# Kernel optimization log

Hardware: AMD Instinct MI355X
Metric: run time of the kernel (lower is better)

## Reference

```python
import jax, jax.numpy as jnp
import numpy as np

N = 50000   # nodes
E = 400000  # edges
IN = 32     # in_channel
M = 64      # mid_channel
L = 3       # num_layers
EPS = 1e-5


def layer_norm(x, g, b):
    mu = jnp.mean(x, axis=-1, keepdims=True)
    var = jnp.mean((x - mu) ** 2, axis=-1, keepdims=True)
    return (x - mu) / jnp.sqrt(var + EPS) * g + b


def setup_inputs() -> dict:
    key = jax.random.key(0)
    ks = jax.random.split(key, 14)
    s = 0.05
    return {
        "x": jax.random.normal(ks[0], (N, IN), jnp.float32),
        "edge_index": jax.random.randint(ks[1], (2, E), 0, N, jnp.int64),
        # node encoder: Linear(IN->M) + LayerNorm(M)
        "enc_W": jax.random.normal(ks[2], (IN, M), jnp.float32) * s,
        "enc_b": jnp.zeros((M,), jnp.float32),
        "enc_g": jnp.ones((M,), jnp.float32),
        "enc_beta": jnp.zeros((M,), jnp.float32),
        # per-layer pre-norm
        "ln_g": jnp.ones((L, M), jnp.float32),
        "ln_b": jnp.zeros((L, M), jnp.float32),
        # SAGEConvV2 edge MLP: Linear(2M->2M) -> ReLU -> Linear(2M->M)
        "W1": jax.random.normal(ks[3], (L, 2 * M, 2 * M), jnp.float32) * s,
        "b1": jnp.zeros((L, 2 * M), jnp.float32),
        "W2": jax.random.normal(ks[4], (L, 2 * M, M), jnp.float32) * s,
        "b2": jnp.zeros((L, M), jnp.float32),
        # root weight lin_r: Linear(M->M, bias=False)
        "Wr": jax.random.normal(ks[5], (L, M, M), jnp.float32) * s,
    }


def reference(x, edge_index, enc_W, enc_b, enc_g, enc_beta,
              ln_g, ln_b, W1, b1, W2, b2, Wr):
    src = edge_index[0]  # x_j source nodes
    dst = edge_index[1]  # x_i target nodes (aggregation index)
    # node encoder
    x = layer_norm(x @ enc_W + enc_b, enc_g, enc_beta)
    # mean-aggregation denominator (in-degree, clamped to 1 like PyG scatter-mean)
    deg = jax.ops.segment_sum(jnp.ones((E,), x.dtype), dst, num_segments=N)
    deg = jnp.maximum(deg, 1.0)[:, None]
    for l in range(L):  # small fixed layer count
        # res+ block: norm -> act -> (dropout: identity in eval) -> conv -> residual
        h = jax.nn.relu(layer_norm(x, ln_g[l], ln_b[l]))
        # message: concat([x_i, x_j]) -> 2-layer MLP   [E, 2M] -> [E, M]
        msg = jnp.concatenate([h[dst], h[src]], axis=-1)
        msg = jax.nn.relu(msg @ W1[l] + b1[l]) @ W2[l] + b2[l]
        # scatter-mean aggregate at target nodes
        agg = jax.ops.segment_sum(msg, dst, num_segments=N) / deg
        # root weight
        h = agg + h @ Wr[l]
        x = x + h
    return x
```

## Files before the change

kernel.cpp:

```cpp
#include <hip/hip_runtime.h>
#include <hip/hip_bf16.h>

#define N_NODES 50000
#define N_EDGES 400000
#define IN_CH 32
#define EPS 1e-5f
#define SCAN_NB ((N_NODES + 1023) / 1024)
#define EL_CAP 384

#define HIST_B ((N_EDGES + 255) / 256)
#define WCT_TOT (3 * 320 * 64)
#define W2T_TOT (3 * 64 * 128)
#define RPK_B ((WCT_TOT + W2T_TOT + 255) / 256)
#define ENC_B ((N_NODES + 63) / 64)

typedef __attribute__((ext_vector_type(8))) short bh8;
typedef __attribute__((ext_vector_type(4))) float fx4;
typedef __attribute__((ext_vector_type(2))) float fx2;

static __device__ __forceinline__ unsigned int f2bf(float f) {
    __hip_bfloat16 h = __float2bfloat16(f);
    return (unsigned int)*(unsigned short*)&h;
}
static __device__ __forceinline__ unsigned short f2bfu(float f) {
    __hip_bfloat16 h = __float2bfloat16(f);
    return *(unsigned short*)&h;
}
static __device__ __forceinline__ float bflo(unsigned int u) { return __uint_as_float(u << 16); }

__global__ __launch_bounds__(256) void setup_kernel(
    const int* __restrict__ ei, int* __restrict__ cnt,
    const float* __restrict__ W1, const float* __restrict__ Wr,
    const float* __restrict__ W2,
    unsigned short* __restrict__ WcT, unsigned short* __restrict__ W2T,
    const float* __restrict__ x, const float* __restrict__ encW,
    const float* __restrict__ encb, const float* __restrict__ encg,
    const float* __restrict__ encbeta, float* __restrict__ xout) {
    int b = blockIdx.x;
    if (b < HIST_B) {
        int e = b * 256 + threadIdx.x;
        if (e < N_EDGES) atomicAdd(&cnt[ei[N_EDGES + e]], 1);
        return;
    }
    b -= HIST_B;
    if (b < RPK_B) {
        int t = b * 256 + threadIdx.x;
        if (t < WCT_TOT) {
            int l = t / (320 * 64);
            int rem = t % (320 * 64);
            int j = rem / 64, c = rem % 64;
            float v;
            if (j < 128)      v = W1[(l * 128 + c) * 128 + j];
            else if (j < 256) v = W1[(l * 128 + 64 + c) * 128 + (j - 128)];
            else              v = Wr[(l * 64 + c) * 64 + (j - 256)];
            WcT[t] = f2bfu(v);
        } else if (t < WCT_TOT + W2T_TOT) {
            int t2 = t - WCT_TOT;
            int l = t2 / 8192, rem = t2 % 8192;
            int n = rem / 128, k = rem % 128;
            W2T[t2] = f2bfu(W2[l * 8192 + k * 64 + n]);
        }
        return;
    }
    b -= RPK_B;
    __shared__ unsigned short wT[64 * 32];
    int tid = threadIdx.x;
    for (int t = tid; t < IN_CH * 64; t += 256) {
        int k = t >> 6, c = t & 63;
        wT[c * 32 + k] = f2bfu(encW[t]);
    }
    __syncthreads();
    int lane = tid & 63, wid = tid >> 6;
    int l15 = lane & 15, g4 = lane >> 4;
    int node0 = b * 64 + wid * 16;
    int arow = min(node0 + l15, N_NODES - 1);
    float4 xa = *(const float4*)(x + (size_t)arow * 32 + g4 * 8);
    float4 xb = *(const float4*)(x + (size_t)arow * 32 + g4 * 8 + 4);
    bh8 af;
    af[0] = (short)f2bfu(xa.x); af[1] = (short)f2bfu(xa.y);
    af[2] = (short)f2bfu(xa.z); af[3] = (short)f2bfu(xa.w);
    af[4] = (short)f2bfu(xb.x); af[5] = (short)f2bfu(xb.y);
    af[6] = (short)f2bfu(xb.z); af[7] = (short)f2bfu(xb.w);
    float cb[4], gvv[4], bvv[4];
    fx4 cf[4];
    #pragma unroll
    for (int nb = 0; nb < 4; ++nb) {
        int cc = nb * 16 + l15;
        cb[nb] = encb[cc]; gvv[nb] = encg[cc]; bvv[nb] = encbeta[cc];
        bh8 bf = *(const bh8*)&wT[(nb * 16 + l15) * 32 + g4 * 8];
        cf[nb] = __builtin_amdgcn_mfma_f32_16x16x32_bf16(
            af, bf, (fx4){0.f, 0.f, 0.f, 0.f}, 0, 0, 0);
    }
    float vals[4][4];
    #pragma unroll
    for (int nb = 0; nb < 4; ++nb)
        #pragma unroll
        for (int r = 0; r < 4; ++r) vals[nb][r] = cf[nb][r] + cb[nb];
    #pragma unroll
    for (int r = 0; r < 4; ++r) {
        float s = vals[0][r] + vals[1][r] + vals[2][r] + vals[3][r];
        s += __shfl_xor(s, 1, 16);
        s += __shfl_xor(s, 2, 16);
        s += __shfl_xor(s, 4, 16);
        s += __shfl_xor(s, 8, 16);
        float mu = s * (1.f / 64.f);
        float q = 0.f;
        #pragma unroll
        for (int nb = 0; nb < 4; ++nb) { float d = vals[nb][r] - mu; q += d * d; }
        q += __shfl_xor(q, 1, 16);
        q += __shfl_xor(q, 2, 16);
        q += __shfl_xor(q, 4, 16);
        q += __shfl_xor(q, 8, 16);
        float rs = rsqrtf(q * (1.f / 64.f) + EPS);
        int nd = node0 + g4 * 4 + r;
        if (nd < N_NODES) {
            #pragma unroll
            for (int nb = 0; nb < 4; ++nb)
                xout[(size_t)nd * 64 + nb * 16 + l15] =
                    (vals[nb][r] - mu) * rs * gvv[nb] + bvv[nb];
        }
    }
}

__global__ __launch_bounds__(1024) void scan1_kernel(const int* __restrict__ cnt,
                                                     int* __restrict__ exw,
                                                     int* __restrict__ bsum) {
    int b = blockIdx.x, t = threadIdx.x;
    int i = b * 1024 + t;
    int v = (i < N_NODES) ? cnt[i] : 0;
    int lane = t & 63, w = t >> 6;
    int s = v;
    #pragma unroll
    for (int off = 1; off < 64; off <<= 1) {
        int u = __shfl_up(s, off, 64);
        if (lane >= off) s += u;
    }
    __shared__ int ws[16];
    if (lane == 63) ws[w] = s;
    __syncthreads();
    if (t < 16) {
        int sv = ws[t];
        #pragma unroll
        for (int off = 1; off < 16; off <<= 1) {
            int u = __shfl_up(sv, off, 64);
            if (lane >= off) sv += u;
        }
        ws[t] = sv;
    }
    __syncthreads();
    int prefix = (w > 0) ? ws[w - 1] : 0;
    int incl = s + prefix;
    if (i < N_NODES) exw[i] = incl - v;
    if (t == 1023) bsum[b] = incl;
}

__global__ __launch_bounds__(1024) void scan3_kernel(const int* __restrict__ exw,
                                                     const int* __restrict__ bsum,
                                                     int* __restrict__ rp,
                                                     int* __restrict__ cnt) {
    __shared__ int pfx;
    __shared__ int total;
    int b = blockIdx.x, t = threadIdx.x;
    if (t < 64) {
        int v = (t < SCAN_NB) ? bsum[t] : 0;
        #pragma unroll
        for (int off = 1; off < 64; off <<= 1) {
            int u = __shfl_up(v, off, 64);
            if (t >= off) v += u;
        }
        if (b == 0 && t == 0) pfx = 0;
        if (b > 0 && t == b - 1) pfx = v;
        if (t == SCAN_NB - 1) total = v;
    }
    __syncthreads();
    int i = b * 1024 + t;
    if (i < N_NODES) {
        rp[i] = exw[i] + pfx;
        cnt[i] = 0;
    }
    if (b == 0 && t == 0) rp[N_NODES] = total;
}

__global__ void fill_kernel(const int* __restrict__ ei, const int* __restrict__ rp,
                            int* __restrict__ cur, int* __restrict__ el) {
    int e = blockIdx.x * 256 + threadIdx.x;
    if (e < N_EDGES) {
        int d = ei[N_EDGES + e];
        int p = atomicAdd(&cur[d], 1);
        el[rp[d] + p] = ei[e];
    }
}

__global__ __launch_bounds__(256, 8) void fused10_kernel(
    float* __restrict__ x, float* __restrict__ xR,
    const unsigned char* __restrict__ A8I, const unsigned char* __restrict__ B8I,
    const unsigned short* __restrict__ W2T, const float* __restrict__ b2,
    const int* __restrict__ rp, const int* __restrict__ el,
    const float* __restrict__ g, const float* __restrict__ bvec,
    const unsigned short* __restrict__ WcT, const float* __restrict__ b1,
    unsigned char* __restrict__ A8O, unsigned char* __restrict__ B8O, int mode) {
    __shared__ float bufF[1088];
    __shared__ unsigned int slds[16][68];
    __shared__ int el_lds[EL_CAP];
    __shared__ int rp_lds[17];
    float* slds_f = (float*)slds;
    int tid = threadIdx.x;
    int lane = tid & 63, wid = tid >> 6;
    int l15 = lane & 15, g4 = lane >> 4;
    int base = blockIdx.x * 16;
    unsigned int* hU = (unsigned int*)bufF;
    int n = tid >> 4, sq = tid & 15;

    int col = wid * 16 + l15;
    int nd_l = base + g4 * 4;

    if (mode != 0) {
        if (tid < 17) rp_lds[tid] = rp[min(base + tid, N_NODES)];
        __syncthreads();
        int e0 = rp_lds[0];
        int nE = rp_lds[16] - e0;
        bool inl = (nE <= EL_CAP);
        if (inl) for (int t = tid; t < nE; t += 256) el_lds[t] = el[e0 + t];

        int nd_g = base + n;
        float av[8], acc[8];
        {
            uint2 a0 = *(const uint2*)(A8I + (size_t)min(nd_g, N_NODES - 1) * 128 + sq * 8);
            fx2 d0 = __builtin_amdgcn_cvt_pk_f32_fp8((int)a0.x, false);
            fx2 d1 = __builtin_amdgcn_cvt_pk_f32_fp8((int)a0.x, true);
            fx2 d2 = __builtin_amdgcn_cvt_pk_f32_fp8((int)a0.y, false);
            fx2 d3 = __builtin_amdgcn_cvt_pk_f32_fp8((int)a0.y, true);
            av[0] = d0.x; av[1] = d0.y; av[2] = d1.x; av[3] = d1.y;
            av[4] = d2.x; av[5] = d2.y; av[6] = d3.x; av[7] = d3.y;
        }
        #pragma unroll
        for (int i = 0; i < 8; ++i) acc[i] = 0.f;

        float xpre[4];
        #pragma unroll
        for (int r = 0; r < 4; ++r) {
            int nd = min(nd_l + r, N_NODES - 1);
            xpre[r] = xR[(size_t)nd * 64 + col];
        }
        __syncthreads();

        int es = rp_lds[n] - e0, ee = rp_lds[n + 1] - e0;
        int e2 = es;
        int cn = ee - e2; if (cn > 8) cn = 8;
        uint2 bufv[8];
        #pragma unroll
        for (int j = 0; j < 8; ++j)
            if (j < cn) {
                int src = inl ? el_lds[e2 + j] : el[e0 + e2 + j];
                bufv[j] = *(const uint2*)(B8I + (size_t)src * 128 + sq * 8);
            }
        while (cn > 0) {
            #pragma unroll
            for (int j = 0; j < 8; ++j)
                if (j < cn) {
                    fx2 f0 = __builtin_amdgcn_cvt_pk_f32_fp8((int)bufv[j].x, false);
                    fx2 f1 = __builtin_amdgcn_cvt_pk_f32_fp8((int)bufv[j].x, true);
                    fx2 f2 = __builtin_amdgcn_cvt_pk_f32_fp8((int)bufv[j].y, false);
                    fx2 f3 = __builtin_amdgcn_cvt_pk_f32_fp8((int)bufv[j].y, true);
                    acc[0] += fmaxf(av[0] + f0.x, 0.f);
                    acc[1] += fmaxf(av[1] + f0.y, 0.f);
                    acc[2] += fmaxf(av[2] + f1.x, 0.f);
                    acc[3] += fmaxf(av[3] + f1.y, 0.f);
                    acc[4] += fmaxf(av[4] + f2.x, 0.f);
                    acc[5] += fmaxf(av[5] + f2.y, 0.f);
                    acc[6] += fmaxf(av[6] + f3.x, 0.f);
                    acc[7] += fmaxf(av[7] + f3.y, 0.f);
                }
            e2 += cn;
            cn = ee - e2; if (cn > 8) cn = 8;
            #pragma unroll
            for (int j = 0; j < 8; ++j)
                if (j < cn) {
                    int src = inl ? el_lds[e2 + j] : el[e0 + e2 + j];
                    bufv[j] = *(const uint2*)(B8I + (size_t)src * 128 + sq * 8);
                }
        }
        #pragma unroll
        for (int jj = 0; jj < 4; ++jj)
            slds[n][sq * 4 + jj] = f2bf(acc[2 * jj]) | (f2bf(acc[2 * jj + 1]) << 16);
        __syncthreads();

        bh8 sa[4];
        #pragma unroll
        for (int ks = 0; ks < 4; ++ks)
            sa[ks] = *(const bh8*)&slds[l15][ks * 16 + g4 * 4];
        fx4 accm = (fx4){0.f, 0.f, 0.f, 0.f};
        #pragma unroll
        for (int ks = 0; ks < 4; ++ks) {
            bh8 bf = *(const bh8*)(W2T + ((size_t)(wid * 16 + l15) * 128 + ks * 32 + g4 * 8));
            accm = __builtin_amdgcn_mfma_f32_16x16x32_bf16(sa[ks], bf, accm, 0, 0, 0);
        }
        float b2c = b2[col];
        #pragma unroll
        for (int r = 0; r < 4; ++r) {
            int lcl = g4 * 4 + r;
            int cv = rp_lds[lcl + 1] - rp_lds[lcl];
            float inv = cv > 0 ? 1.f / (float)cv : 0.f;
            float msk = cv > 0 ? 1.f : 0.f;
            float xn = xpre[r] + accm[r] * inv + b2c * msk;
            if (mode == 2) x[(size_t)(nd_l + r) * 64 + col] = xn;
            else           bufF[lcl * 68 + col] = xn;
        }
        if (mode == 2) return;
        __syncthreads();
    }

    {
        float vv[4];
        if (mode == 0) {
            int nd = base + n;
            float4 v0 = ((const float4*)(x + (size_t)nd * 64))[sq];
            vv[0] = v0.x; vv[1] = v0.y; vv[2] = v0.z; vv[3] = v0.w;
        } else {
            #pragma unroll
            for (int i = 0; i < 4; ++i) vv[i] = bufF[n * 68 + sq * 4 + i];
        }
        float s = vv[0] + vv[1] + vv[2] + vv[3];
        s += __shfl_xor(s, 1, 16);
        s += __shfl_xor(s, 2, 16);
        s += __shfl_xor(s, 4, 16);
        s += __shfl_xor(s, 8, 16);
        float mu = s * (1.f / 64.f);
        float q = 0.f;
        #pragma unroll
        for (int i = 0; i < 4; ++i) { float d = vv[i] - mu; q += d * d; }
        q += __shfl_xor(q, 1, 16);
        q += __shfl_xor(q, 2, 16);
        q += __shfl_xor(q, 4, 16);
        q += __shfl_xor(q, 8, 16);
        float rs = rsqrtf(q * (1.f / 64.f) + EPS);
        float4 gg = *(const float4*)&g[sq * 4];
        float4 bb = *(const float4*)&bvec[sq * 4];
        float gv[4] = {gg.x, gg.y, gg.z, gg.w};
        float bv[4] = {bb.x, bb.y, bb.z, bb.w};
        __syncthreads();
        #pragma unroll
        for (int i = 0; i < 4; ++i) slds_f[n * 68 + sq * 4 + i] = vv[i];
        #pragma unroll
        for (int jj = 0; jj < 2; ++jj) {
            float h0 = fmaxf((vv[2 * jj] - mu) * rs * gv[2 * jj] + bv[2 * jj], 0.f);
            float h1 = fmaxf((vv[2 * jj + 1] - mu) * rs * gv[2 * jj + 1] + bv[2 * jj + 1], 0.f);
            hU[n * 33 + sq * 2 + jj] = f2bf(h0) | (f2bf(h1) << 16);
        }
    }
    __syncthreads();

    bh8 a2[2];
    #pragma unroll
    for (int ks = 0; ks < 2; ++ks)
        a2[ks] = *(const bh8*)&hU[l15 * 33 + ks * 16 + g4 * 4];
    int ndg = base + g4 * 4;
    #pragma unroll
    for (int nn = 0; nn < 5; ++nn) {
        int nb = wid * 5 + nn;
        fx4 c = (fx4){0.f, 0.f, 0.f, 0.f};
        #pragma unroll
        for (int ks = 0; ks < 2; ++ks) {
            bh8 bf = *(const bh8*)(WcT + ((size_t)(nb * 16 + l15) * 64 + ks * 32 + g4 * 8));
            c = __builtin_amdgcn_mfma_f32_16x16x32_bf16(a2[ks], bf, c, 0, 0, 0);
        }
        int colw = nb * 16 + l15;
        #pragma unroll
        for (int r = 0; r < 4; ++r) {
            int nd = ndg + r;
            float v = c[r];
            if (colw < 128) {
                unsigned int p = __builtin_amdgcn_cvt_pk_fp8_f32(v + b1[colw], 0.f, 0, false);
                A8O[(size_t)nd * 128 + colw] = (unsigned char)(p & 0xFF);
            } else if (colw < 256) {
                unsigned int p = __builtin_amdgcn_cvt_pk_fp8_f32(v, 0.f, 0, false);
                B8O[(size_t)nd * 128 + (colw - 128)] = (unsigned char)(p & 0xFF);
            } else {
                int c2 = colw - 256;
                xR[(size_t)nd * 64 + c2] = slds_f[(g4 * 4 + r) * 68 + c2] + v;
            }
        }
    }
}

extern "C" void kernel_launch(void* const* d_in, const int* in_sizes, int n_in,
                              void* d_out, int out_size, void* d_ws, size_t ws_size,
                              hipStream_t stream) {
    const float* x       = (const float*)d_in[0];
    const int*   ei      = (const int*)d_in[1];
    const float* encW    = (const float*)d_in[2];
    const float* encb    = (const float*)d_in[3];
    const float* encg    = (const float*)d_in[4];
    const float* encbeta = (const float*)d_in[5];
    const float* lng     = (const float*)d_in[6];
    const float* lnb     = (const float*)d_in[7];
    const float* W1      = (const float*)d_in[8];
    const float* b1      = (const float*)d_in[9];
    const float* W2      = (const float*)d_in[10];
    const float* b2      = (const float*)d_in[11];
    const float* Wr      = (const float*)d_in[12];
    float* xout = (float*)d_out;

    char* ws = (char*)d_ws;
    size_t off = 0;
    auto alloc = [&](size_t bytes) -> void* {
        void* p = ws + off;
        off += (bytes + 255) & ~(size_t)255;
        return p;
    };
    unsigned short* WcT  = (unsigned short*)alloc(3 * 320 * 64 * sizeof(unsigned short));
    unsigned short* W2T  = (unsigned short*)alloc(3 * 64 * 128 * sizeof(unsigned short));
    unsigned char*  A80  = (unsigned char*)alloc((size_t)N_NODES * 128);
    unsigned char*  A81  = (unsigned char*)alloc((size_t)N_NODES * 128);
    unsigned char*  B80  = (unsigned char*)alloc((size_t)N_NODES * 128);
    unsigned char*  B81  = (unsigned char*)alloc((size_t)N_NODES * 128);
    float*          xR   = (float*)alloc((size_t)N_NODES * 64 * sizeof(float));
    int*            cnt  = (int*)alloc(N_NODES * sizeof(int));
    int*            rp   = (int*)alloc((N_NODES + 1) * sizeof(int));
    int*            el   = (int*)alloc(N_EDGES * sizeof(int));
    int*            exw  = (int*)alloc(N_NODES * sizeof(int));
    int*            bsum = (int*)alloc(SCAN_NB * sizeof(int));

    hipMemsetAsync(cnt, 0, N_NODES * sizeof(int), stream);
    setup_kernel<<<HIST_B + RPK_B + ENC_B, 256, 0, stream>>>(
        ei, cnt, W1, Wr, W2, WcT, W2T, x, encW, encb, encg, encbeta, xout);
    scan1_kernel<<<SCAN_NB, 1024, 0, stream>>>(cnt, exw, bsum);
    scan3_kernel<<<SCAN_NB, 1024, 0, stream>>>(exw, bsum, rp, cnt);
    fill_kernel<<<(N_EDGES + 255) / 256, 256, 0, stream>>>(ei, rp, cnt, el);

    int gblocks = (N_NODES + 15) / 16;
    fused10_kernel<<<gblocks, 256, 0, stream>>>(
        xout, xR, A80, B80, W2T, b2, rp, el, lng, lnb,
        WcT, b1, A80, B80, 0);
    fused10_kernel<<<gblocks, 256, 0, stream>>>(
        xout, xR, A80, B80, W2T, b2, rp, el, lng + 64, lnb + 64,
        WcT + (size_t)1 * 320 * 64, b1 + 128, A81, B81, 1);
    fused10_kernel<<<gblocks, 256, 0, stream>>>(
        xout, xR, A81, B81, W2T + (size_t)1 * 64 * 128, b2 + 64, rp, el, lng + 128, lnb + 128,
        WcT + (size_t)2 * 320 * 64, b1 + 256, A80, B80, 1);
    fused10_kernel<<<gblocks, 256, 0, stream>>>(
        xout, xR, A80, B80, W2T + (size_t)2 * 64 * 128, b2 + 128, rp, el, lng, lnb,
        WcT, b1, A81, B81, 2);
}
```

Before: 194.9 us.

## Merge CSR fill into first layer kernel and use persistent grid-stride tiles

The edge-list fill kernel is folded into the mode-0 layer kernel: the first FILL_B blocks do the atomic fill and the rest run the encoder-side projection, removing one launch. All layer kernels now launch a fixed grid of 2048 blocks that loop over 16-node tiles. The gather batch is raised from 8 to 12 edges in flight per thread. The tail bounds clamps are dropped because N is an exact multiple of 16. More registers per thread from the larger gather buffer could reduce occupancy. The persistent loop also adds extra barriers per tile.

```diff
diff --git a/kernel.cpp b/kernel.cpp
--- a/kernel.cpp
+++ b/kernel.cpp
@@ -7,8 +7,11 @@
 #define EPS 1e-5f
 #define SCAN_NB ((N_NODES + 1023) / 1024)
 #define EL_CAP 384
+#define NTILES (N_NODES / 16)
+#define PGRID 2048
 
 #define HIST_B ((N_EDGES + 255) / 256)
+#define FILL_B ((N_EDGES + 255) / 256)
 #define WCT_TOT (3 * 320 * 64)
 #define W2T_TOT (3 * 64 * 128)
 #define RPK_B ((WCT_TOT + W2T_TOT + 255) / 256)
@@ -181,205 +184,211 @@
     if (b == 0 && t == 0) rp[N_NODES] = total;
 }
 
-__global__ void fill_kernel(const int* __restrict__ ei, const int* __restrict__ rp,
-                            int* __restrict__ cur, int* __restrict__ el) {
-    int e = blockIdx.x * 256 + threadIdx.x;
-    if (e < N_EDGES) {
-        int d = ei[N_EDGES + e];
-        int p = atomicAdd(&cur[d], 1);
-        el[rp[d] + p] = ei[e];
-    }
-}
-
-__global__ __launch_bounds__(256, 8) void fused10_kernel(
+__global__ __launch_bounds__(256, 8) void fused11_kernel(
     float* __restrict__ x, float* __restrict__ xR,
     const unsigned char* __restrict__ A8I, const unsigned char* __restrict__ B8I,
     const unsigned short* __restrict__ W2T, const float* __restrict__ b2,
-    const int* __restrict__ rp, const int* __restrict__ el,
+    const int* __restrict__ rp, int* __restrict__ el,
     const float* __restrict__ g, const float* __restrict__ bvec,
     const unsigned short* __restrict__ WcT, const float* __restrict__ b1,
-    unsigned char* __restrict__ A8O, unsigned char* __restrict__ B8O, int mode) {
+    unsigned char* __restrict__ A8O, unsigned char* __restrict__ B8O,
+    int mode, const int* __restrict__ ei, int* __restrict__ cur, int fill_blocks) {
     __shared__ float bufF[1088];
     __shared__ unsigned int slds[16][68];
     __shared__ int el_lds[EL_CAP];
     __shared__ int rp_lds[17];
     float* slds_f = (float*)slds;
     int tid = threadIdx.x;
+
+    if (mode == 0 && blockIdx.x < fill_blocks) {
+        int e = blockIdx.x * 256 + tid;
+        if (e < N_EDGES) {
+            int d = ei[N_EDGES + e];
+            int p = atomicAdd(&cur[d], 1);
+            el[rp[d] + p] = ei[e];
+        }
+        return;
+    }
+    int bstart = (mode == 0) ? (blockIdx.x - fill_blocks) : blockIdx.x;
+    int bstride = (mode == 0) ? (gridDim.x - fill_blocks) : gridDim.x;
+
     int lane = tid & 63, wid = tid >> 6;
     int l15 = lane & 15, g4 = lane >> 4;
-    int base = blockIdx.x * 16;
     unsigned int* hU = (unsigned int*)bufF;
     int n = tid >> 4, sq = tid & 15;
-
     int col = wid * 16 + l15;
-    int nd_l = base + g4 * 4;
-
-    if (mode != 0) {
-        if (tid < 17) rp_lds[tid] = rp[min(base + tid, N_NODES)];
-        __syncthreads();
-        int e0 = rp_lds[0];
-        int nE = rp_lds[16] - e0;
-        bool inl = (nE <= EL_CAP);
-        if (inl) for (int t = tid; t < nE; t += 256) el_lds[t] = el[e0 + t];
-
-        int nd_g = base + n;
-        float av[8], acc[8];
-        {
-            uint2 a0 = *(const uint2*)(A8I + (size_t)min(nd_g, N_NODES - 1) * 128 + sq * 8);
-            fx2 d0 = __builtin_amdgcn_cvt_pk_f32_fp8((int)a0.x, false);
-            fx2 d1 = __builtin_amdgcn_cvt_pk_f32_fp8((int)a0.x, true);
-            fx2 d2 = __builtin_amdgcn_cvt_pk_f32_fp8((int)a0.y, false);
-            fx2 d3 = __builtin_amdgcn_cvt_pk_f32_fp8((int)a0.y, true);
-            av[0] = d0.x; av[1] = d0.y; av[2] = d1.x; av[3] = d1.y;
-            av[4] = d2.x; av[5] = d2.y; av[6] = d3.x; av[7] = d3.y;
-        }
-        #pragma unroll
-        for (int i = 0; i < 8; ++i) acc[i] = 0.f;
-
-        float xpre[4];
-        #pragma unroll
-        for (int r = 0; r < 4; ++r) {
-            int nd = min(nd_l + r, N_NODES - 1);
-            xpre[r] = xR[(size_t)nd * 64 + col];
-        }
-        __syncthreads();
-
-        int es = rp_lds[n] - e0, ee = rp_lds[n + 1] - e0;
-        int e2 = es;
-        int cn = ee - e2; if (cn > 8) cn = 8;
-        uint2 bufv[8];
-        #pragma unroll
-        for (int j = 0; j < 8; ++j)
-            if (j < cn) {
-                int src = inl ? el_lds[e2 + j] : el[e0 + e2 + j];
-                bufv[j] = *(const uint2*)(B8I + (size_t)src * 128 + sq * 8);
-            }
-        while (cn > 0) {
-            #pragma unroll
-            for (int j = 0; j < 8; ++j)
-                if (j < cn) {
-                    fx2 f0 = __builtin_amdgcn_cvt_pk_f32_fp8((int)bufv[j].x, false);
-                    fx2 f1 = __builtin_amdgcn_cvt_pk_f32_fp8((int)bufv[j].x, true);
-                    fx2 f2 = __builtin_amdgcn_cvt_pk_f32_fp8((int)bufv[j].y, false);
-                    fx2 f3 = __builtin_amdgcn_cvt_pk_f32_fp8((int)bufv[j].y, true);
-                    acc[0] += fmaxf(av[0] + f0.x, 0.f);
-                    acc[1] += fmaxf(av[1] + f0.y, 0.f);
-                    acc[2] += fmaxf(av[2] + f1.x, 0.f);
-                    acc[3] += fmaxf(av[3] + f1.y, 0.f);
-                    acc[4] += fmaxf(av[4] + f2.x, 0.f);
-                    acc[5] += fmaxf(av[5] + f2.y, 0.f);
-                    acc[6] += fmaxf(av[6] + f3.x, 0.f);
-                    acc[7] += fmaxf(av[7] + f3.y, 0.f);
-                }
-            e2 += cn;
-            cn = ee - e2; if (cn > 8) cn = 8;
-            #pragma unroll
-            for (int j = 0; j < 8; ++j)
+
+    for (int tb = bstart; tb < NTILES; tb += bstride) {
+        int base = tb * 16;
+        int nd_l = base + g4 * 4;
+
+        if (mode != 0) {
+            if (tid < 17) rp_lds[tid] = rp[base + tid];
+            __syncthreads();
+            int e0 = rp_lds[0];
+            int nE = rp_lds[16] - e0;
+            bool inl = (nE <= EL_CAP);
+            if (inl) for (int t = tid; t < nE; t += 256) el_lds[t] = el[e0 + t];
+
+            int nd_g = base + n;
+            float av[8], acc[8];
+            {
+                uint2 a0 = *(const uint2*)(A8I + (size_t)nd_g * 128 + sq * 8);
+                fx2 d0 = __builtin_amdgcn_cvt_pk_f32_fp8((int)a0.x, false);
+                fx2 d1 = __builtin_amdgcn_cvt_pk_f32_fp8((int)a0.x, true);
+                fx2 d2 = __builtin_amdgcn_cvt_pk_f32_fp8((int)a0.y, false);
+                fx2 d3 = __builtin_amdgcn_cvt_pk_f32_fp8((int)a0.y, true);
+                av[0] = d0.x; av[1] = d0.y; av[2] = d1.x; av[3] = d1.y;
+                av[4] = d2.x; av[5] = d2.y; av[6] = d3.x; av[7] = d3.y;
+            }
+            #pragma unroll
+            for (int i = 0; i < 8; ++i) acc[i] = 0.f;
+
+            float xpre[4];
+            #pragma unroll
+            for (int r = 0; r < 4; ++r)
+                xpre[r] = xR[(size_t)(nd_l + r) * 64 + col];
+            __syncthreads();
+
+            int es = rp_lds[n] - e0, ee = rp_lds[n + 1] - e0;
+            int e2 = es;
+            int cn = ee - e2; if (cn > 12) cn = 12;
+            uint2 bufv[12];
+            #pragma unroll
+            for (int j = 0; j < 12; ++j)
                 if (j < cn) {
                     int src = inl ? el_lds[e2 + j] : el[e0 + e2 + j];
                     bufv[j] = *(const uint2*)(B8I + (size_t)src * 128 + sq * 8);
                 }
-        }
-        #pragma unroll
-        for (int jj = 0; jj < 4; ++jj)
-            slds[n][sq * 4 + jj] = f2bf(acc[2 * jj]) | (f2bf(acc[2 * jj + 1]) << 16);
+            while (cn > 0) {
+                #pragma unroll
+                for (int j = 0; j < 12; ++j)
+                    if (j < cn) {
+                        fx2 f0 = __builtin_amdgcn_cvt_pk_f32_fp8((int)bufv[j].x, false);
+                        fx2 f1 = __builtin_amdgcn_cvt_pk_f32_fp8((int)bufv[j].x, true);
+                        fx2 f2 = __builtin_amdgcn_cvt_pk_f32_fp8((int)bufv[j].y, false);
+                        fx2 f3 = __builtin_amdgcn_cvt_pk_f32_fp8((int)bufv[j].y, true);
+                        acc[0] += fmaxf(av[0] + f0.x, 0.f);
+                        acc[1] += fmaxf(av[1] + f0.y, 0.f);
+                        acc[2] += fmaxf(av[2] + f1.x, 0.f);
+                        acc[3] += fmaxf(av[3] + f1.y, 0.f);
+                        acc[4] += fmaxf(av[4] + f2.x, 0.f);
+                        acc[5] += fmaxf(av[5] + f2.y, 0.f);
+                        acc[6] += fmaxf(av[6] + f3.x, 0.f);
+                        acc[7] += fmaxf(av[7] + f3.y, 0.f);
+                    }
+                e2 += cn;
+                cn = ee - e2; if (cn > 12) cn = 12;
+                #pragma unroll
+                for (int j = 0; j < 12; ++j)
+                    if (j < cn) {
+                        int src = inl ? el_lds[e2 + j] : el[e0 + e2 + j];
+                        bufv[j] = *(const uint2*)(B8I + (size_t)src * 128 + sq * 8);
+                    }
+            }
+            #pragma unroll
+            for (int jj = 0; jj < 4; ++jj)
+                slds[n][sq * 4 + jj] = f2bf(acc[2 * jj]) | (f2bf(acc[2 * jj + 1]) << 16);
+            __syncthreads();
+
+            bh8 sa[4];
+            #pragma unroll
+            for (int ks = 0; ks < 4; ++ks)
+                sa[ks] = *(const bh8*)&slds[l15][ks * 16 + g4 * 4];
+            fx4 accm = (fx4){0.f, 0.f, 0.f, 0.f};
+            #pragma unroll
+            for (int ks = 0; ks < 4; ++ks) {
+                bh8 bf = *(const bh8*)(W2T + ((size_t)(wid * 16 + l15) * 128 + ks * 32 + g4 * 8));
+                accm = __builtin_amdgcn_mfma_f32_16x16x32_bf16(sa[ks], bf, accm, 0, 0, 0);
+            }
+            float b2c = b2[col];
+            #pragma unroll
+            for (int r = 0; r < 4; ++r) {
+                int lcl = g4 * 4 + r;
+                int cv = rp_lds[lcl + 1] - rp_lds[lcl];
+                float inv = cv > 0 ? 1.f / (float)cv : 0.f;
+                float msk = cv > 0 ? 1.f : 0.f;
+                float xn = xpre[r] + accm[r] * inv + b2c * msk;
+                if (mode == 2) x[(size_t)(nd_l + r) * 64 + col] = xn;
+                else           bufF[lcl * 68 + col] = xn;
+            }
+        }
+
+        if (mode != 2) {
+            if (mode != 0) __syncthreads();
+            {
+                float vv[4];
+                if (mode == 0) {
+                    int nd = base + n;
+                    float4 v0 = ((const float4*)(x + (size_t)nd * 64))[sq];
+                    vv[0] = v0.x; vv[1] = v0.y; vv[2] = v0.z; vv[3] = v0.w;
+                } else {
+                    #pragma unroll
+                    for (int i = 0; i < 4; ++i) vv[i] = bufF[n * 68 + sq * 4 + i];
+                }
+                float s = vv[0] + vv[1] + vv[2] + vv[3];
+                s += __shfl_xor(s, 1, 16);
+                s += __shfl_xor(s, 2, 16);
+                s += __shfl_xor(s, 4, 16);
+                s += __shfl_xor(s, 8, 16);
+                float mu = s * (1.f / 64.f);
+                float q = 0.f;
+                #pragma unroll
+                for (int i = 0; i < 4; ++i) { float d = vv[i] - mu; q += d * d; }
+                q += __shfl_xor(q, 1, 16);
+                q += __shfl_xor(q, 2, 16);
+                q += __shfl_xor(q, 4, 16);
+                q += __shfl_xor(q, 8, 16);
+                float rs = rsqrtf(q * (1.f / 64.f) + EPS);
+                float4 gg = *(const float4*)&g[sq * 4];
+                float4 bb = *(const float4*)&bvec[sq * 4];
+                float gv[4] = {gg.x, gg.y, gg.z, gg.w};
+                float bv[4] = {bb.x, bb.y, bb.z, bb.w};
+                __syncthreads();
+                #pragma unroll
+                for (int i = 0; i < 4; ++i) slds_f[n * 68 + sq * 4 + i] = vv[i];
+                #pragma unroll
+                for (int jj = 0; jj < 2; ++jj) {
+                    float h0 = fmaxf((vv[2 * jj] - mu) * rs * gv[2 * jj] + bv[2 * jj], 0.f);
+                    float h1 = fmaxf((vv[2 * jj + 1] - mu) * rs * gv[2 * jj + 1] + bv[2 * jj + 1], 0.f);
+                    hU[n * 33 + sq * 2 + jj] = f2bf(h0) | (f2bf(h1) << 16);
+                }
+            }
+            __syncthreads();
+
+            bh8 a2[2];
+            #pragma unroll
+            for (int ks = 0; ks < 2; ++ks)
+                a2[ks] = *(const bh8*)&hU[l15 * 33 + ks * 16 + g4 * 4];
+            int ndg = base + g4 * 4;
+            #pragma unroll
+            for (int nn = 0; nn < 5; ++nn) {
+                int nb = wid * 5 + nn;
+                fx4 c = (fx4){0.f, 0.f, 0.f, 0.f};
+                #pragma unroll
+                for (int ks = 0; ks < 2; ++ks) {
+                    bh8 bf = *(const bh8*)(WcT + ((size_t)(nb * 16 + l15) * 64 + ks * 32 + g4 * 8));
+                    c = __builtin_amdgcn_mfma_f32_16x16x32_bf16(a2[ks], bf, c, 0, 0, 0);
+                }
+                int colw = nb * 16 + l15;
+                #pragma unroll
+                for (int r = 0; r < 4; ++r) {
+                    int nd = ndg + r;
+                    float v = c[r];
+                    if (colw < 128) {
+                        unsigned int p = __builtin_amdgcn_cvt_pk_fp8_f32(v + b1[colw], 0.f, 0, false);
+                        A8O[(size_t)nd * 128 + colw] = (unsigned char)(p & 0xFF);
+                    } else if (colw < 256) {
+                        unsigned int p = __builtin_amdgcn_cvt_pk_fp8_f32(v, 0.f, 0, false);
+                        B8O[(size_t)nd * 128 + (colw - 128)] = (unsigned char)(p & 0xFF);
+                    } else {
+                        int c2 = colw - 256;
+                        xR[(size_t)nd * 64 + c2] = slds_f[(g4 * 4 + r) * 68 + c2] + v;
+                    }
+                }
+            }
+        }
         __syncthreads();
-
-        bh8 sa[4];
-        #pragma unroll
-        for (int ks = 0; ks < 4; ++ks)
-            sa[ks] = *(const bh8*)&slds[l15][ks * 16 + g4 * 4];
-        fx4 accm = (fx4){0.f, 0.f, 0.f, 0.f};
-        #pragma unroll
-        for (int ks = 0; ks < 4; ++ks) {
-            bh8 bf = *(const bh8*)(W2T + ((size_t)(wid * 16 + l15) * 128 + ks * 32 + g4 * 8));
-            accm = __builtin_amdgcn_mfma_f32_16x16x32_bf16(sa[ks], bf, accm, 0, 0, 0);
-        }
-        float b2c = b2[col];
-        #pragma unroll
-        for (int r = 0; r < 4; ++r) {
-            int lcl = g4 * 4 + r;
-            int cv = rp_lds[lcl + 1] - rp_lds[lcl];
-            float inv = cv > 0 ? 1.f / (float)cv : 0.f;
-            float msk = cv > 0 ? 1.f : 0.f;
-            float xn = xpre[r] + accm[r] * inv + b2c * msk;
-            if (mode == 2) x[(size_t)(nd_l + r) * 64 + col] = xn;
-            else           bufF[lcl * 68 + col] = xn;
-        }
-        if (mode == 2) return;
-        __syncthreads();
-    }
-
-    {
-        float vv[4];
-        if (mode == 0) {
-            int nd = base + n;
-            float4 v0 = ((const float4*)(x + (size_t)nd * 64))[sq];
-            vv[0] = v0.x; vv[1] = v0.y; vv[2] = v0.z; vv[3] = v0.w;
-        } else {
-            #pragma unroll
-            for (int i = 0; i < 4; ++i) vv[i] = bufF[n * 68 + sq * 4 + i];
-        }
-        float s = vv[0] + vv[1] + vv[2] + vv[3];
-        s += __shfl_xor(s, 1, 16);
-        s += __shfl_xor(s, 2, 16);
-        s += __shfl_xor(s, 4, 16);
-        s += __shfl_xor(s, 8, 16);
-        float mu = s * (1.f / 64.f);
-        float q = 0.f;
-        #pragma unroll
-        for (int i = 0; i < 4; ++i) { float d = vv[i] - mu; q += d * d; }
-        q += __shfl_xor(q, 1, 16);
-        q += __shfl_xor(q, 2, 16);
-        q += __shfl_xor(q, 4, 16);
-        q += __shfl_xor(q, 8, 16);
-        float rs = rsqrtf(q * (1.f / 64.f) + EPS);
-        float4 gg = *(const float4*)&g[sq * 4];
-        float4 bb = *(const float4*)&bvec[sq * 4];
-        float gv[4] = {gg.x, gg.y, gg.z, gg.w};
-        float bv[4] = {bb.x, bb.y, bb.z, bb.w};
-        __syncthreads();
-        #pragma unroll
-        for (int i = 0; i < 4; ++i) slds_f[n * 68 + sq * 4 + i] = vv[i];
-        #pragma unroll
-        for (int jj = 0; jj < 2; ++jj) {
-            float h0 = fmaxf((vv[2 * jj] - mu) * rs * gv[2 * jj] + bv[2 * jj], 0.f);
-            float h1 = fmaxf((vv[2 * jj + 1] - mu) * rs * gv[2 * jj + 1] + bv[2 * jj + 1], 0.f);
-            hU[n * 33 + sq * 2 + jj] = f2bf(h0) | (f2bf(h1) << 16);
-        }
-    }
-    __syncthreads();
-
-    bh8 a2[2];
-    #pragma unroll
-    for (int ks = 0; ks < 2; ++ks)
-        a2[ks] = *(const bh8*)&hU[l15 * 33 + ks * 16 + g4 * 4];
-    int ndg = base + g4 * 4;
-    #pragma unroll
-    for (int nn = 0; nn < 5; ++nn) {
-        int nb = wid * 5 + nn;
-        fx4 c = (fx4){0.f, 0.f, 0.f, 0.f};
-        #pragma unroll
-        for (int ks = 0; ks < 2; ++ks) {
-            bh8 bf = *(const bh8*)(WcT + ((size_t)(nb * 16 + l15) * 64 + ks * 32 + g4 * 8));
-            c = __builtin_amdgcn_mfma_f32_16x16x32_bf16(a2[ks], bf, c, 0, 0, 0);
-        }
-        int colw = nb * 16 + l15;
-        #pragma unroll
-        for (int r = 0; r < 4; ++r) {
-            int nd = ndg + r;
-            float v = c[r];
-            if (colw < 128) {
-                unsigned int p = __builtin_amdgcn_cvt_pk_fp8_f32(v + b1[colw], 0.f, 0, false);
-                A8O[(size_t)nd * 128 + colw] = (unsigned char)(p & 0xFF);
-            } else if (colw < 256) {
-                unsigned int p = __builtin_amdgcn_cvt_pk_fp8_f32(v, 0.f, 0, false);
-                B8O[(size_t)nd * 128 + (colw - 128)] = (unsigned char)(p & 0xFF);
-            } else {
-                int c2 = colw - 256;
-                xR[(size_t)nd * 64 + c2] = slds_f[(g4 * 4 + r) * 68 + c2] + v;
-            }
-        }
     }
 }
 
@@ -426,19 +435,17 @@
         ei, cnt, W1, Wr, W2, WcT, W2T, x, encW, encb, encg, encbeta, xout);
     scan1_kernel<<<SCAN_NB, 1024, 0, stream>>>(cnt, exw, bsum);
     scan3_kernel<<<SCAN_NB, 1024, 0, stream>>>(exw, bsum, rp, cnt);
-    fill_kernel<<<(N_EDGES + 255) / 256, 256, 0, stream>>>(ei, rp, cnt, el);
-
-    int gblocks = (N_NODES + 15) / 16;
-    fused10_kernel<<<gblocks, 256, 0, stream>>>(
+
+    fused11_kernel<<<FILL_B + PGRID, 256, 0, stream>>>(
         xout, xR, A80, B80, W2T, b2, rp, el, lng, lnb,
-        WcT, b1, A80, B80, 0);
-    fused10_kernel<<<gblocks, 256, 0, stream>>>(
+        WcT, b1, A80, B80, 0, ei, cnt, FILL_B);
+    fused11_kernel<<<PGRID, 256, 0, stream>>>(
         xout, xR, A80, B80, W2T, b2, rp, el, lng + 64, lnb + 64,
-        WcT + (size_t)1 * 320 * 64, b1 + 128, A81, B81, 1);
-    fused10_kernel<<<gblocks, 256, 0, stream>>>(
+        WcT + (size_t)1 * 320 * 64, b1 + 128, A81, B81, 1, ei, cnt, 0);
+    fused11_kernel<<<PGRID, 256, 0, stream>>>(
         xout, xR, A81, B81, W2T + (size_t)1 * 64 * 128, b2 + 64, rp, el, lng + 128, lnb + 128,
-        WcT + (size_t)2 * 320 * 64, b1 + 256, A80, B80, 1);
-    fused10_kernel<<<gblocks, 256, 0, stream>>>(
+        WcT + (size_t)2 * 320 * 64, b1 + 256, A80, B80, 1, ei, cnt, 0);
+    fused11_kernel<<<PGRID, 256, 0, stream>>>(
         xout, xR, A80, B80, W2T + (size_t)2 * 64 * 128, b2 + 128, rp, el, lng, lnb,
-        WcT, b1, A81, B81, 2);
-}
+        WcT, b1, A81, B81, 2, ei, cnt, 0);
+}
```

Result: slower. 433.5 us (+122.4%).

## Halve nodes per block to eight and use 32 threads per node

Applied to the files above, without the earlier changes.

Each block of the fused layer kernel now handles 8 nodes instead of 16. There are 32 threads per node, each gathering 4 fp8 bytes per edge instead of 8. The grid doubles, each node's gather and LayerNorm are split over more lanes, and the unused half of the 16-row MFMA tiles is zero-padded. This aims for more parallelism and memory-level concurrency in the edge gather. The cost is half-wasted MFMA rows, more zero-fill work, and more per-block overhead.

```diff
diff --git a/kernel.cpp b/kernel.cpp
--- a/kernel.cpp
+++ b/kernel.cpp
@@ -6,7 +6,8 @@
 #define IN_CH 32
 #define EPS 1e-5f
 #define SCAN_NB ((N_NODES + 1023) / 1024)
-#define EL_CAP 384
+#define EL_CAP 256
+#define TILE_N 8
 
 #define HIST_B ((N_EDGES + 255) / 256)
 #define WCT_TOT (3 * 320 * 64)
@@ -26,7 +27,6 @@
     __hip_bfloat16 h = __float2bfloat16(f);
     return *(unsigned short*)&h;
 }
-static __device__ __forceinline__ float bflo(unsigned int u) { return __uint_as_float(u << 16); }
 
 __global__ __launch_bounds__(256) void setup_kernel(
     const int* __restrict__ ei, int* __restrict__ cnt,
@@ -191,7 +191,7 @@
     }
 }
 
-__global__ __launch_bounds__(256, 8) void fused10_kernel(
+__global__ __launch_bounds__(256, 8) void fused13_kernel(
     float* __restrict__ x, float* __restrict__ xR,
     const unsigned char* __restrict__ A8I, const unsigned char* __restrict__ B8I,
     const unsigned short* __restrict__ W2T, const float* __restrict__ b2,
@@ -202,44 +202,41 @@
     __shared__ float bufF[1088];
     __shared__ unsigned int slds[16][68];
     __shared__ int el_lds[EL_CAP];
-    __shared__ int rp_lds[17];
+    __shared__ int rp_lds[9];
     float* slds_f = (float*)slds;
     int tid = threadIdx.x;
     int lane = tid & 63, wid = tid >> 6;
     int l15 = lane & 15, g4 = lane >> 4;
-    int base = blockIdx.x * 16;
+    int base = blockIdx.x * TILE_N;
     unsigned int* hU = (unsigned int*)bufF;
-    int n = tid >> 4, sq = tid & 15;
-
+    int n = tid >> 5, sq = tid & 31;
     int col = wid * 16 + l15;
-    int nd_l = base + g4 * 4;
 
     if (mode != 0) {
-        if (tid < 17) rp_lds[tid] = rp[min(base + tid, N_NODES)];
+        if (tid < 9) rp_lds[tid] = rp[base + tid];
+        for (int t = tid; t < 8 * 68; t += 256) ((unsigned int*)slds)[8 * 68 + t] = 0u;
         __syncthreads();
         int e0 = rp_lds[0];
-        int nE = rp_lds[16] - e0;
+        int nE = rp_lds[8] - e0;
         bool inl = (nE <= EL_CAP);
         if (inl) for (int t = tid; t < nE; t += 256) el_lds[t] = el[e0 + t];
 
         int nd_g = base + n;
-        float av[8], acc[8];
+        float av[4], acc[4];
         {
-            uint2 a0 = *(const uint2*)(A8I + (size_t)min(nd_g, N_NODES - 1) * 128 + sq * 8);
-            fx2 d0 = __builtin_amdgcn_cvt_pk_f32_fp8((int)a0.x, false);
-            fx2 d1 = __builtin_amdgcn_cvt_pk_f32_fp8((int)a0.x, true);
-            fx2 d2 = __builtin_amdgcn_cvt_pk_f32_fp8((int)a0.y, false);
-            fx2 d3 = __builtin_amdgcn_cvt_pk_f32_fp8((int)a0.y, true);
+            unsigned int a0 = *(const unsigned int*)(A8I + (size_t)nd_g * 128 + sq * 4);
+            fx2 d0 = __builtin_amdgcn_cvt_pk_f32_fp8((int)a0, false);
+            fx2 d1 = __builtin_amdgcn_cvt_pk_f32_fp8((int)a0, true);
             av[0] = d0.x; av[1] = d0.y; av[2] = d1.x; av[3] = d1.y;
-            av[4] = d2.x; av[5] = d2.y; av[6] = d3.x; av[7] = d3.y;
-        }
-        #pragma unroll
-        for (int i = 0; i < 8; ++i) acc[i] = 0.f;
+        }
+        #pragma unroll
+        for (int i = 0; i < 4; ++i) acc[i] = 0.f;
 
         float xpre[4];
         #pragma unroll
         for (int r = 0; r < 4; ++r) {
-            int nd = min(nd_l + r, N_NODES - 1);
+            int lcl = g4 * 4 + r;
+            int nd = base + min(lcl, 7);
             xpre[r] = xR[(size_t)nd * 64 + col];
         }
         __syncthreads();
@@ -247,29 +244,23 @@
         int es = rp_lds[n] - e0, ee = rp_lds[n + 1] - e0;
         int e2 = es;
         int cn = ee - e2; if (cn > 8) cn = 8;
-        uint2 bufv[8];
+        unsigned int bufv[8];
         #pragma unroll
         for (int j = 0; j < 8; ++j)
             if (j < cn) {
                 int src = inl ? el_lds[e2 + j] : el[e0 + e2 + j];
-                bufv[j] = *(const uint2*)(B8I + (size_t)src * 128 + sq * 8);
+                bufv[j] = *(const unsigned int*)(B8I + (size_t)src * 128 + sq * 4);
             }
         while (cn > 0) {
             #pragma unroll
             for (int j = 0; j < 8; ++j)
                 if (j < cn) {
-                    fx2 f0 = __builtin_amdgcn_cvt_pk_f32_fp8((int)bufv[j].x, false);
-                    fx2 f1 = __builtin_amdgcn_cvt_pk_f32_fp8((int)bufv[j].x, true);
-                    fx2 f2 = __builtin_amdgcn_cvt_pk_f32_fp8((int)bufv[j].y, false);
-                    fx2 f3 = __builtin_amdgcn_cvt_pk_f32_fp8((int)bufv[j].y, true);
+                    fx2 f0 = __builtin_amdgcn_cvt_pk_f32_fp8((int)bufv[j], false);
+                    fx2 f1 = __builtin_amdgcn_cvt_pk_f32_fp8((int)bufv[j], true);
                     acc[0] += fmaxf(av[0] + f0.x, 0.f);
                     acc[1] += fmaxf(av[1] + f0.y, 0.f);
                     acc[2] += fmaxf(av[2] + f1.x, 0.f);
                     acc[3] += fmaxf(av[3] + f1.y, 0.f);
-                    acc[4] += fmaxf(av[4] + f2.x, 0.f);
-                    acc[5] += fmaxf(av[5] + f2.y, 0.f);
-                    acc[6] += fmaxf(av[6] + f3.x, 0.f);
-                    acc[7] += fmaxf(av[7] + f3.y, 0.f);
                 }
             e2 += cn;
             cn = ee - e2; if (cn > 8) cn = 8;
@@ -277,12 +268,11 @@
             for (int j = 0; j < 8; ++j)
                 if (j < cn) {
                     int src = inl ? el_lds[e2 + j] : el[e0 + e2 + j];
-                    bufv[j] = *(const uint2*)(B8I + (size_t)src * 128 + sq * 8);
+                    bufv[j] = *(const unsigned int*)(B8I + (size_t)src * 128 + sq * 4);
                 }
         }
-        #pragma unroll
-        for (int jj = 0; jj < 4; ++jj)
-            slds[n][sq * 4 + jj] = f2bf(acc[2 * jj]) | (f2bf(acc[2 * jj + 1]) << 16);
+        slds[n][sq * 2 + 0] = f2bf(acc[0]) | (f2bf(acc[1]) << 16);
+        slds[n][sq * 2 + 1] = f2bf(acc[2]) | (f2bf(acc[3]) << 16);
         __syncthreads();
 
         bh8 sa[4];
@@ -299,54 +289,53 @@
         #pragma unroll
         for (int r = 0; r < 4; ++r) {
             int lcl = g4 * 4 + r;
-            int cv = rp_lds[lcl + 1] - rp_lds[lcl];
-            float inv = cv > 0 ? 1.f / (float)cv : 0.f;
-            float msk = cv > 0 ? 1.f : 0.f;
-            float xn = xpre[r] + accm[r] * inv + b2c * msk;
-            if (mode == 2) x[(size_t)(nd_l + r) * 64 + col] = xn;
-            else           bufF[lcl * 68 + col] = xn;
+            if (lcl < 8) {
+                int cv = rp_lds[lcl + 1] - rp_lds[lcl];
+                float inv = cv > 0 ? 1.f / (float)cv : 0.f;
+                float msk = cv > 0 ? 1.f : 0.f;
+                float xn = xpre[r] + accm[r] * inv + b2c * msk;
+                if (mode == 2) x[(size_t)(base + lcl) * 64 + col] = xn;
+                else           bufF[lcl * 68 + col] = xn;
+            }
         }
         if (mode == 2) return;
         __syncthreads();
     }
 
     {
-        float vv[4];
+        float vv[2];
         if (mode == 0) {
             int nd = base + n;
-            float4 v0 = ((const float4*)(x + (size_t)nd * 64))[sq];
-            vv[0] = v0.x; vv[1] = v0.y; vv[2] = v0.z; vv[3] = v0.w;
+            float2 v0 = ((const float2*)(x + (size_t)nd * 64))[sq];
+            vv[0] = v0.x; vv[1] = v0.y;
         } else {
-            #pragma unroll
-            for (int i = 0; i < 4; ++i) vv[i] = bufF[n * 68 + sq * 4 + i];
-        }
-        float s = vv[0] + vv[1] + vv[2] + vv[3];
-        s += __shfl_xor(s, 1, 16);
-        s += __shfl_xor(s, 2, 16);
-        s += __shfl_xor(s, 4, 16);
-        s += __shfl_xor(s, 8, 16);
+            vv[0] = bufF[n * 68 + sq * 2 + 0];
+            vv[1] = bufF[n * 68 + sq * 2 + 1];
+        }
+        float s = vv[0] + vv[1];
+        s += __shfl_xor(s, 1, 32);
+        s += __shfl_xor(s, 2, 32);
+        s += __shfl_xor(s, 4, 32);
+        s += __shfl_xor(s, 8, 32);
+        s += __shfl_xor(s, 16, 32);
         float mu = s * (1.f / 64.f);
-        float q = 0.f;
-        #pragma unroll
-        for (int i = 0; i < 4; ++i) { float d = vv[i] - mu; q += d * d; }
-        q += __shfl_xor(q, 1, 16);
-        q += __shfl_xor(q, 2, 16);
-        q += __shfl_xor(q, 4, 16);
-        q += __shfl_xor(q, 8, 16);
+        float d0 = vv[0] - mu, d1 = vv[1] - mu;
+        float q = d0 * d0 + d1 * d1;
+        q += __shfl_xor(q, 1, 32);
+        q += __shfl_xor(q, 2, 32);
+        q += __shfl_xor(q, 4, 32);
+        q += __shfl_xor(q, 8, 32);
+        q += __shfl_xor(q, 16, 32);
         float rs = rsqrtf(q * (1.f / 64.f) + EPS);
-        float4 gg = *(const float4*)&g[sq * 4];
-        float4 bb = *(const float4*)&bvec[sq * 4];
-        float gv[4] = {gg.x, gg.y, gg.z, gg.w};
-        float bv[4] = {bb.x, bb.y, bb.z, bb.w};
+        float2 gg = *(const float2*)&g[sq * 2];
+        float2 bb = *(const float2*)&bvec[sq * 2];
         __syncthreads();
-        #pragma unroll
-        for (int i = 0; i < 4; ++i) slds_f[n * 68 + sq * 4 + i] = vv[i];
-        #pragma unroll
-        for (int jj = 0; jj < 2; ++jj) {
-            float h0 = fmaxf((vv[2 * jj] - mu) * rs * gv[2 * jj] + bv[2 * jj], 0.f);
-            float h1 = fmaxf((vv[2 * jj + 1] - mu) * rs * gv[2 * jj + 1] + bv[2 * jj + 1], 0.f);
-            hU[n * 33 + sq * 2 + jj] = f2bf(h0) | (f2bf(h1) << 16);
-        }
+        slds_f[n * 68 + sq * 2 + 0] = vv[0];
+        slds_f[n * 68 + sq * 2 + 1] = vv[1];
+        float h0 = fmaxf((vv[0] - mu) * rs * gg.x + bb.x, 0.f);
+        float h1 = fmaxf((vv[1] - mu) * rs * gg.y + bb.y, 0.f);
+        hU[n * 33 + sq] = f2bf(h0) | (f2bf(h1) << 16);
+        for (int t = tid; t < 8 * 33; t += 256) hU[8 * 33 + t] = 0u;
     }
     __syncthreads();
 
@@ -354,7 +343,6 @@
     #pragma unroll
     for (int ks = 0; ks < 2; ++ks)
         a2[ks] = *(const bh8*)&hU[l15 * 33 + ks * 16 + g4 * 4];
-    int ndg = base + g4 * 4;
     #pragma unroll
     for (int nn = 0; nn < 5; ++nn) {
         int nb = wid * 5 + nn;
@@ -367,7 +355,9 @@
         int colw = nb * 16 + l15;
         #pragma unroll
         for (int r = 0; r < 4; ++r) {
-            int nd = ndg + r;
+            int lcl = g4 * 4 + r;
+            if (lcl >= 8) continue;
+            int nd = base + lcl;
             float v = c[r];
             if (colw < 128) {
                 unsigned int p = __builtin_amdgcn_cvt_pk_fp8_f32(v + b1[colw], 0.f, 0, false);
@@ -377,7 +367,7 @@
                 B8O[(size_t)nd * 128 + (colw - 128)] = (unsigned char)(p & 0xFF);
             } else {
                 int c2 = colw - 256;
-                xR[(size_t)nd * 64 + c2] = slds_f[(g4 * 4 + r) * 68 + c2] + v;
+                xR[(size_t)nd * 64 + c2] = slds_f[lcl * 68 + c2] + v;
             }
         }
     }
@@ -428,17 +418,17 @@
     scan3_kernel<<<SCAN_NB, 1024, 0, stream>>>(exw, bsum, rp, cnt);
     fill_kernel<<<(N_EDGES + 255) / 256, 256, 0, stream>>>(ei, rp, cnt, el);
 
-    int gblocks = (N_NODES + 15) / 16;
-    fused10_kernel<<<gblocks, 256, 0, stream>>>(
+    int gblocks = N_NODES / TILE_N;
+    fused13_kernel<<<gblocks, 256, 0, stream>>>(
         xout, xR, A80, B80, W2T, b2, rp, el, lng, lnb,
         WcT, b1, A80, B80, 0);
-    fused10_kernel<<<gblocks, 256, 0, stream>>>(
+    fused13_kernel<<<gblocks, 256, 0, stream>>>(
         xout, xR, A80, B80, W2T, b2, rp, el, lng + 64, lnb + 64,
         WcT + (size_t)1 * 320 * 64, b1 + 128, A81, B81, 1);
-    fused10_kernel<<<gblocks, 256, 0, stream>>>(
+    fused13_kernel<<<gblocks, 256, 0, stream>>>(
         xout, xR, A81, B81, W2T + (size_t)1 * 64 * 128, b2 + 64, rp, el, lng + 128, lnb + 128,
         WcT + (size_t)2 * 320 * 64, b1 + 256, A80, B80, 1);
-    fused10_kernel<<<gblocks, 256, 0, stream>>>(
+    fused13_kernel<<<gblocks, 256, 0, stream>>>(
         xout, xR, A80, B80, W2T + (size_t)2 * 64 * 128, b2 + 128, rp, el, lng, lnb,
         WcT, b1, A81, B81, 2);
 }
```

New measurement: 268.9 us. 1.38x slower.
